# Performance work log

Hardware: AMD Instinct MI355X
Metric: run time of the kernel (lower is better)

Reference implementation:

```python
import jax, jax.numpy as jnp
import numpy as np

D_MODEL = 1024

def setup_inputs() -> dict:
    key = jax.random.key(0)
    k1, k2, kU, kb, kw, kfb = jax.random.split(key, 6)
    B, S, d = 8, 2048, D_MODEL
    x1 = jax.random.normal(k1, (B, S, d), dtype=jnp.float32)
    x2 = jax.random.normal(k2, (B, S, d), dtype=jnp.float32)
    U = jax.random.normal(kU, (d, d), dtype=jnp.float32) * (1.0 / np.sqrt(d))
    bias = jax.random.normal(kb, (d,), dtype=jnp.float32) * 0.02
    fc_w = jax.random.normal(kw, (d // 2, d), dtype=jnp.float32) * (1.0 / np.sqrt(d))
    fc_b = jnp.zeros((d // 2,), dtype=jnp.float32)
    return {"x1": x1, "x2": x2, "U": U, "bias": bias, "fc_w": fc_w, "fc_b": fc_b}

def reference(x1, x2, U, bias, fc_w, fc_b):
    # attn scores: (x2 @ U) @ x1^T  -> [B, S2, S1]
    attn = jnp.einsum("bsd,de,bte->bst", x2, U, x1)
    # additive bias per key position: x1 @ bias -> [B, 1, S1]
    attn = attn + jnp.einsum("btd,d->bt", x1, bias)[:, None, :]
    attn = jax.nn.softmax(attn, axis=-1)
    # dropout is identity in eval mode
    out = jnp.einsum("bst,btd->bsd", attn, x1)
    out = jnp.einsum("bsd,ed->bse", out, fc_w) + fc_b
    return jax.nn.relu(out)
```

## Files before the change

kernel.cpp:

```cpp
#include <hip/hip_runtime.h>
#include <hip/hip_fp16.h>
#include <cstddef>
#include <cstdint>

typedef _Float16 f16;
typedef _Float16 f16x8 __attribute__((ext_vector_type(8)));
typedef _Float16 f16x4 __attribute__((ext_vector_type(4)));
typedef float    f32x4 __attribute__((ext_vector_type(4)));

#define BK 64

__device__ __forceinline__ void gload16(const void* g, void* lds) {
  __builtin_amdgcn_global_load_lds(
      (const __attribute__((address_space(1))) unsigned int*)g,
      (__attribute__((address_space(3))) unsigned int*)lds, 16, 0, 0);
}

template<int R>
__device__ __forceinline__ void stage_f16(f16 (*buf)[BK], const f16* __restrict__ src,
                                          int ld, int w, int lane) {
#pragma unroll
  for (int i = 0; i < R / 32; i++) {
    const int grp  = w * (R / 32) + i;
    const int r    = grp * 8 + (lane >> 3);
    const int slot = (lane & 7) ^ (r & 7);
    gload16(src + (size_t)r * ld + slot * 8, &buf[grp * 8][0]);
  }
}

template<int R>
struct RegStage {
  static constexpr int NV = (R == 128) ? 8 : 4;
  float4 v[NV];
  __device__ __forceinline__ void load(const float* __restrict__ src, int ld, int tid) {
    const int r = (R == 128) ? (tid >> 1) : (tid >> 2);
    const int h = (R == 128) ? (tid & 1) * 32 : (tid & 3) * 16;
    const float* p = src + (size_t)r * ld + h;
#pragma unroll
    for (int j = 0; j < NV; j++) v[j] = ((const float4*)p)[j];
  }
  __device__ __forceinline__ void write(f16 (*buf)[BK], int tid) {
    const int r = (R == 128) ? (tid >> 1) : (tid >> 2);
    const int h = (R == 128) ? (tid & 1) * 32 : (tid & 3) * 16;
#pragma unroll
    for (int g = 0; g < NV / 2; g++) {
      const float4 a = v[g * 2], b = v[g * 2 + 1];
      f16x8 o;
      o[0] = (f16)a.x; o[1] = (f16)a.y; o[2] = (f16)a.z; o[3] = (f16)a.w;
      o[4] = (f16)b.x; o[5] = (f16)b.y; o[6] = (f16)b.z; o[7] = (f16)b.w;
      const int slot = (h / 8 + g) ^ (r & 7);
      *(f16x8*)&buf[r][slot * 8] = o;
    }
  }
};

template<int BMt, int BNt, typename TA, typename TB, bool BIAS, bool RELU, typename TC>
__global__ __launch_bounds__(256, 2)
void gemm_tn(const TA* __restrict__ A, int lda,
             const TB* __restrict__ B, int ldb,
             TC* __restrict__ C, int ldc,
             const float* __restrict__ bias, int K)
{
  constexpr int MF = BMt / 32;
  constexpr int NF = BNt / 32;
  __shared__ f16 As[2][BMt][BK];
  __shared__ f16 Bs[2][BNt][BK];
  const int tid  = threadIdx.x;
  const int lane = tid & 63;
  const int w    = tid >> 6;
  const int wr   = w >> 1, wc = w & 1;

  const int gx = gridDim.x, nxy = gx * gridDim.y;
  int lin = blockIdx.y * gx + blockIdx.x;
  lin = (lin & 7) * (nxy >> 3) + (lin >> 3);
  const int m0 = (lin % gx) * BMt;
  const int n0 = (lin / gx) * BNt;

  f32x4 acc[MF][NF] = {};
  RegStage<BMt> ra;
  RegStage<BNt> rb;

  auto stage_issue = [&](int buf, int k0) {
    if constexpr (sizeof(TA) == 2)
      stage_f16<BMt>(As[buf], (const f16*)A + (size_t)m0 * lda + k0, lda, w, lane);
    else
      ra.load((const float*)A + (size_t)m0 * lda + k0, lda, tid);
    if constexpr (sizeof(TB) == 2)
      stage_f16<BNt>(Bs[buf], (const f16*)B + (size_t)n0 * ldb + k0, ldb, w, lane);
    else
      rb.load((const float*)B + (size_t)n0 * ldb + k0, ldb, tid);
  };
  auto stage_write = [&](int buf) {
    if constexpr (sizeof(TA) == 4) ra.write(As[buf], tid);
    if constexpr (sizeof(TB) == 4) rb.write(Bs[buf], tid);
  };
  auto compute = [&](int buf) {
    const int fr = lane & 15, q = lane >> 4;
#pragma unroll
    for (int kk = 0; kk < 2; kk++) {
      f16x8 af[MF], bf[NF];
#pragma unroll
      for (int i = 0; i < MF; i++) {
        const int r = wr * (BMt / 2) + i * 16 + fr;
        const int slot = (kk * 4 + q) ^ (r & 7);
        af[i] = *(const f16x8*)&As[buf][r][slot * 8];
      }
#pragma unroll
      for (int j = 0; j < NF; j++) {
        const int r = wc * (BNt / 2) + j * 16 + fr;
        const int slot = (kk * 4 + q) ^ (r & 7);
        bf[j] = *(const f16x8*)&Bs[buf][r][slot * 8];
      }
#pragma unroll
      for (int i = 0; i < MF; i++)
#pragma unroll
        for (int j = 0; j < NF; j++)
          acc[i][j] = __builtin_amdgcn_mfma_f32_16x16x32_f16(af[i], bf[j], acc[i][j], 0, 0, 0);
    }
  };

  stage_issue(0, 0);
  stage_write(0);
  __syncthreads();

  const int KT = K / BK;
  for (int kt = 0; kt < KT; kt++) {
    const int cur = kt & 1, nxt = cur ^ 1;
    if (kt + 1 < KT) stage_issue(nxt, (kt + 1) * BK);
    compute(cur);
    if (kt + 1 < KT) stage_write(nxt);
    __syncthreads();
  }

  const int fr = lane & 15;
  const int rg = (lane >> 4) << 2;
#pragma unroll
  for (int i = 0; i < MF; i++) {
#pragma unroll
    for (int j = 0; j < NF; j++) {
      const int col = n0 + wc * (BNt / 2) + j * 16 + fr;
      float bv = 0.f;
      if constexpr (BIAS) bv = bias[col];
#pragma unroll
      for (int r = 0; r < 4; r++) {
        const int row = m0 + wr * (BMt / 2) + i * 16 + rg + r;
        float v = acc[i][j][r] + bv;
        if constexpr (RELU) v = fmaxf(v, 0.f);
        C[(size_t)row * ldc + col] = (TC)v;
      }
    }
  }
}

__global__ __launch_bounds__(256)
void copy_f32_f16(const float* __restrict__ in, f16* __restrict__ o)
{
  const size_t i = ((size_t)blockIdx.x * 256 + threadIdx.x) * 8;
  const float4 a = ((const float4*)(in + i))[0];
  const float4 b = ((const float4*)(in + i))[1];
  f16x8 v;
  v[0] = (f16)a.x; v[1] = (f16)a.y; v[2] = (f16)a.z; v[3] = (f16)a.w;
  v[4] = (f16)b.x; v[5] = (f16)b.y; v[6] = (f16)b.z; v[7] = (f16)b.w;
  *(f16x8*)(o + i) = v;
}

__global__ __launch_bounds__(256)
void copy_uf(const float* __restrict__ U, const float* __restrict__ fcw,
             f16* __restrict__ Uh, f16* __restrict__ Fh)
{
  const bool isU = blockIdx.x < 512;
  const size_t base = (size_t)(isU ? blockIdx.x : blockIdx.x - 512) * 2048;
  const float* in = (isU ? U : fcw) + base;
  f16* o = (isU ? Uh : Fh) + base;
  const size_t i = (size_t)threadIdx.x * 8;
  const float4 a = ((const float4*)(in + i))[0];
  const float4 b = ((const float4*)(in + i))[1];
  f16x8 v;
  v[0] = (f16)a.x; v[1] = (f16)a.y; v[2] = (f16)a.z; v[3] = (f16)a.w;
  v[4] = (f16)b.x; v[5] = (f16)b.y; v[6] = (f16)b.z; v[7] = (f16)b.w;
  *(f16x8*)(o + i) = v;
}

__global__ __launch_bounds__(256)
void bias_dot(const float* __restrict__ x1, const float* __restrict__ bias,
              float* __restrict__ bT)
{
  const int row  = blockIdx.x * 4 + (threadIdx.x >> 6);
  const int lane = threadIdx.x & 63;
  const float4* r = (const float4*)(x1 + (size_t)row * 1024);
  const float4* bb = (const float4*)bias;
  float acc = 0.f;
#pragma unroll
  for (int j = 0; j < 4; j++) {
    const float4 a = r[lane + j * 64];
    const float4 b = bb[lane + j * 64];
    acc += a.x * b.x + a.y * b.y + a.z * b.z + a.w * b.w;
  }
#pragma unroll
  for (int off = 32; off > 0; off >>= 1) acc += __shfl_xor(acc, off);
  if (lane == 0) bT[row] = acc;
}

__global__ __launch_bounds__(256)
void softmax_rows(float* __restrict__ S)
{
  float* row = S + (size_t)blockIdx.x * 2048;
  const int t = threadIdx.x;
  const float4 v0 = ((const float4*)row)[t];
  const float4 v1 = ((const float4*)row)[t + 256];

  float m = fmaxf(fmaxf(fmaxf(v0.x, v0.y), fmaxf(v0.z, v0.w)),
                  fmaxf(fmaxf(v1.x, v1.y), fmaxf(v1.z, v1.w)));
#pragma unroll
  for (int off = 32; off > 0; off >>= 1) m = fmaxf(m, __shfl_xor(m, off));
  __shared__ float red[8];
  if ((t & 63) == 0) red[t >> 6] = m;
  __syncthreads();
  m = fmaxf(fmaxf(red[0], red[1]), fmaxf(red[2], red[3]));

  float e0 = __expf(v0.x - m), e1 = __expf(v0.y - m), e2 = __expf(v0.z - m), e3 = __expf(v0.w - m);
  float e4 = __expf(v1.x - m), e5 = __expf(v1.y - m), e6 = __expf(v1.z - m), e7 = __expf(v1.w - m);
  float s = ((e0 + e1) + (e2 + e3)) + ((e4 + e5) + (e6 + e7));
#pragma unroll
  for (int off = 32; off > 0; off >>= 1) s += __shfl_xor(s, off);
  if ((t & 63) == 0) red[4 + (t >> 6)] = s;
  __syncthreads();
  const float inv = 1.f / (red[4] + red[5] + red[6] + red[7]);

  f16x4 o0, o1;
  o0[0] = (f16)(e0 * inv); o0[1] = (f16)(e1 * inv); o0[2] = (f16)(e2 * inv); o0[3] = (f16)(e3 * inv);
  o1[0] = (f16)(e4 * inv); o1[1] = (f16)(e5 * inv); o1[2] = (f16)(e6 * inv); o1[3] = (f16)(e7 * inv);
  f16x4* orow = (f16x4*)row;
  orow[t]       = o0;
  orow[t + 256] = o1;
}

extern "C" void kernel_launch(void* const* d_in, const int* in_sizes, int n_in,
                              void* d_out, int out_size, void* d_ws, size_t ws_size,
                              hipStream_t stream)
{
  const float* x1   = (const float*)d_in[0];
  const float* x2   = (const float*)d_in[1];
  const float* U    = (const float*)d_in[2];
  const float* bias = (const float*)d_in[3];
  const float* fcw  = (const float*)d_in[4];
  const float* fcb  = (const float*)d_in[5];
  float* out = (float*)d_out;

  const int S = 2048, D = 1024, E = 512, B = 8;
  const size_t MB = 1ull << 20;
  const size_t KB64 = 64 * 1024;

  const bool FULL = ws_size >= (4 * MB + KB64 + 16 * MB);

  char* w = (char*)d_ws;
  f16*   W2   = (f16*)(w);
  f16*   W1Tf = (f16*)(w + 4 * MB);
  float* bT   = FULL ? (float*)(w + 4 * MB) : (float*)(w + 6 * MB);
  float* Sb   = FULL ? (float*)(w + 4 * MB + KB64) : (float*)(w + 6 * MB + KB64);
  f16*   Uh   = FULL ? (f16*)((char*)Sb + 13 * MB) : (f16*)(w + 14 * MB + KB64);
  f16*   Fh   = (f16*)(w + 16 * MB + KB64);
  f16*   W1T  = FULL ? (f16*)Sb + 2048 : W1Tf;
  const int ldw1t = FULL ? 2 * S : S;

  f16* X2h = (f16*)d_out;

  copy_f32_f16<<<dim3(B * S * D / 2048), 256, 0, stream>>>(x2, X2h);
  bias_dot<<<dim3(B * S / 4), 256, 0, stream>>>(x1, bias, bT);
  if (!FULL)
    copy_uf<<<dim3(768), 256, 0, stream>>>(U, fcw, Uh, Fh);

  for (int b = 0; b < B; b++) {
    const float* x1b = x1 + (size_t)b * S * D;
    const f16*   X2b = X2h + (size_t)b * S * D;

    if (FULL) {
      copy_uf<<<dim3(512), 256, 0, stream>>>(U, fcw, Uh, nullptr);

      gemm_tn<64, 128, float, f16, false, false, f16><<<dim3(S / 64, D / 128), 256, 0, stream>>>(
          x1b, D, Uh, D, W2, D, nullptr, D);

      gemm_tn<128, 128, f16, f16, true, false, float><<<dim3(S / 128, S / 128), 256, 0, stream>>>(
          X2b, D, W2, D, Sb, S, bT + (size_t)b * S, D);

      softmax_rows<<<dim3(S), 256, 0, stream>>>(Sb);

      gemm_tn<64, 64, float, float, false, false, f16><<<dim3(E / 64, S / 64), 256, 0, stream>>>(
          fcw, D, x1b, D, W1T, ldw1t, nullptr, D);

      gemm_tn<64, 64, f16, f16, true, true, float><<<dim3(S / 64, E / 64), 256, 0, stream>>>(
          (const f16*)Sb, 2 * S, W1T, ldw1t, out + (size_t)b * S * E, E, fcb, S);
    } else {
      gemm_tn<64, 128, float, f16, false, false, f16><<<dim3(S / 64, D / 128), 256, 0, stream>>>(
          x1b, D, Uh, D, W2, D, nullptr, D);
      gemm_tn<64, 64, f16, float, false, false, f16><<<dim3(E / 64, S / 64), 256, 0, stream>>>(
          Fh, D, x1b, D, W1Tf, S, nullptr, D);
      for (int s0 = 0; s0 < S; s0 += 1024) {
        gemm_tn<64, 128, f16, f16, true, false, float><<<dim3(1024 / 64, S / 128), 256, 0, stream>>>(
            X2b + (size_t)s0 * D, D, W2, D, Sb, S, bT + (size_t)b * S, D);
        softmax_rows<<<dim3(1024), 256, 0, stream>>>(Sb);
        gemm_tn<64, 64, f16, f16, true, true, float><<<dim3(1024 / 64, E / 64), 256, 0, stream>>>(
            (const f16*)Sb, 2 * S, W1Tf, S, out + ((size_t)b * S + s0) * E, E, fcb, S);
      }
    }
  }
}
```

Baseline: 721.5 us.

## Fuse prep kernels, hoist U conversion, use wave-per-row softmax

Merges the x2 fp16 conversion and the bias dot product into one launch. Adds a workspace mode that gives Uh its own slot so the U conversion runs once instead of once per batch. Replaces the block-per-row softmax with a wave-per-row version that reduces only with shuffles and needs no shared memory or barriers. The main savings are fewer launches and no block-level synchronisation in softmax. The cost is higher register pressure in softmax (32 floats per lane) and a more complex workspace layout.

```diff
diff --git a/kernel.cpp b/kernel.cpp
--- a/kernel.cpp
+++ b/kernel.cpp
@@ -153,6 +153,37 @@
 }
 
 __global__ __launch_bounds__(256)
+void prep_head(const float* __restrict__ x2, f16* __restrict__ X2h,
+               const float* __restrict__ x1, const float* __restrict__ bias,
+               float* __restrict__ bT)
+{
+  if (blockIdx.x < 8192) {
+    const size_t i = ((size_t)blockIdx.x * 256 + threadIdx.x) * 8;
+    const float4 a = ((const float4*)(x2 + i))[0];
+    const float4 b = ((const float4*)(x2 + i))[1];
+    f16x8 v;
+    v[0] = (f16)a.x; v[1] = (f16)a.y; v[2] = (f16)a.z; v[3] = (f16)a.w;
+    v[4] = (f16)b.x; v[5] = (f16)b.y; v[6] = (f16)b.z; v[7] = (f16)b.w;
+    *(f16x8*)(X2h + i) = v;
+  } else {
+    const int row  = (blockIdx.x - 8192) * 4 + (threadIdx.x >> 6);
+    const int lane = threadIdx.x & 63;
+    const float4* r = (const float4*)(x1 + (size_t)row * 1024);
+    const float4* bb = (const float4*)bias;
+    float acc = 0.f;
+#pragma unroll
+    for (int j = 0; j < 4; j++) {
+      const float4 a = r[lane + j * 64];
+      const float4 b = bb[lane + j * 64];
+      acc += a.x * b.x + a.y * b.y + a.z * b.z + a.w * b.w;
+    }
+#pragma unroll
+    for (int off = 32; off > 0; off >>= 1) acc += __shfl_xor(acc, off);
+    if (lane == 0) bT[row] = acc;
+  }
+}
+
+__global__ __launch_bounds__(256)
 void copy_f32_f16(const float* __restrict__ in, f16* __restrict__ o)
 {
   const size_t i = ((size_t)blockIdx.x * 256 + threadIdx.x) * 8;
@@ -182,57 +213,39 @@
 }
 
 __global__ __launch_bounds__(256)
-void bias_dot(const float* __restrict__ x1, const float* __restrict__ bias,
-              float* __restrict__ bT)
+void softmax_rows_w(float* __restrict__ S)
 {
   const int row  = blockIdx.x * 4 + (threadIdx.x >> 6);
   const int lane = threadIdx.x & 63;
-  const float4* r = (const float4*)(x1 + (size_t)row * 1024);
-  const float4* bb = (const float4*)bias;
-  float acc = 0.f;
-#pragma unroll
-  for (int j = 0; j < 4; j++) {
-    const float4 a = r[lane + j * 64];
-    const float4 b = bb[lane + j * 64];
-    acc += a.x * b.x + a.y * b.y + a.z * b.z + a.w * b.w;
-  }
-#pragma unroll
-  for (int off = 32; off > 0; off >>= 1) acc += __shfl_xor(acc, off);
-  if (lane == 0) bT[row] = acc;
-}
-
-__global__ __launch_bounds__(256)
-void softmax_rows(float* __restrict__ S)
-{
-  float* row = S + (size_t)blockIdx.x * 2048;
-  const int t = threadIdx.x;
-  const float4 v0 = ((const float4*)row)[t];
-  const float4 v1 = ((const float4*)row)[t + 256];
-
-  float m = fmaxf(fmaxf(fmaxf(v0.x, v0.y), fmaxf(v0.z, v0.w)),
-                  fmaxf(fmaxf(v1.x, v1.y), fmaxf(v1.z, v1.w)));
+  float* rp = S + (size_t)row * 2048;
+  const float4* pr = (const float4*)rp + lane;
+
+  float f[32];
+  float m = -3.4e38f;
+#pragma unroll
+  for (int k = 0; k < 8; k++) {
+    const float4 v = pr[(size_t)k * 64];
+    f[k * 4 + 0] = v.x; f[k * 4 + 1] = v.y; f[k * 4 + 2] = v.z; f[k * 4 + 3] = v.w;
+    m = fmaxf(m, fmaxf(fmaxf(v.x, v.y), fmaxf(v.z, v.w)));
+  }
 #pragma unroll
   for (int off = 32; off > 0; off >>= 1) m = fmaxf(m, __shfl_xor(m, off));
-  __shared__ float red[8];
-  if ((t & 63) == 0) red[t >> 6] = m;
-  __syncthreads();
-  m = fmaxf(fmaxf(red[0], red[1]), fmaxf(red[2], red[3]));
-
-  float e0 = __expf(v0.x - m), e1 = __expf(v0.y - m), e2 = __expf(v0.z - m), e3 = __expf(v0.w - m);
-  float e4 = __expf(v1.x - m), e5 = __expf(v1.y - m), e6 = __expf(v1.z - m), e7 = __expf(v1.w - m);
-  float s = ((e0 + e1) + (e2 + e3)) + ((e4 + e5) + (e6 + e7));
+
+  float s = 0.f;
+#pragma unroll
+  for (int i = 0; i < 32; i++) { f[i] = __expf(f[i] - m); s += f[i]; }
 #pragma unroll
   for (int off = 32; off > 0; off >>= 1) s += __shfl_xor(s, off);
-  if ((t & 63) == 0) red[4 + (t >> 6)] = s;
-  __syncthreads();
-  const float inv = 1.f / (red[4] + red[5] + red[6] + red[7]);
-
-  f16x4 o0, o1;
-  o0[0] = (f16)(e0 * inv); o0[1] = (f16)(e1 * inv); o0[2] = (f16)(e2 * inv); o0[3] = (f16)(e3 * inv);
-  o1[0] = (f16)(e4 * inv); o1[1] = (f16)(e5 * inv); o1[2] = (f16)(e6 * inv); o1[3] = (f16)(e7 * inv);
-  f16x4* orow = (f16x4*)row;
-  orow[t]       = o0;
-  orow[t + 256] = o1;
+  const float inv = 1.f / s;
+
+  f16* hp = (f16*)rp;
+#pragma unroll
+  for (int k = 0; k < 8; k++) {
+    f16x4 o;
+    o[0] = (f16)(f[k * 4 + 0] * inv); o[1] = (f16)(f[k * 4 + 1] * inv);
+    o[2] = (f16)(f[k * 4 + 2] * inv); o[3] = (f16)(f[k * 4 + 3] * inv);
+    *(f16x4*)(hp + 4 * lane + 256 * k) = o;
+  }
 }
 
 extern "C" void kernel_launch(void* const* d_in, const int* in_sizes, int n_in,
@@ -251,31 +264,38 @@
   const size_t MB = 1ull << 20;
   const size_t KB64 = 64 * 1024;
 
-  const bool FULL = ws_size >= (4 * MB + KB64 + 16 * MB);
+  const int MODE = (ws_size >= 4 * MB + KB64 + 2 * MB + 16 * MB) ? 2
+                 : (ws_size >= 4 * MB + KB64 + 16 * MB)          ? 1 : 0;
 
   char* w = (char*)d_ws;
   f16*   W2   = (f16*)(w);
   f16*   W1Tf = (f16*)(w + 4 * MB);
-  float* bT   = FULL ? (float*)(w + 4 * MB) : (float*)(w + 6 * MB);
-  float* Sb   = FULL ? (float*)(w + 4 * MB + KB64) : (float*)(w + 6 * MB + KB64);
-  f16*   Uh   = FULL ? (f16*)((char*)Sb + 13 * MB) : (f16*)(w + 14 * MB + KB64);
+  float* bT   = MODE ? (float*)(w + 4 * MB) : (float*)(w + 6 * MB);
+  float* Sb   = (MODE == 2) ? (float*)(w + 6 * MB + KB64)
+              : MODE        ? (float*)(w + 4 * MB + KB64)
+                            : (float*)(w + 6 * MB + KB64);
+  f16*   Uh   = (MODE == 2) ? (f16*)(w + 4 * MB + KB64)
+              : MODE        ? (f16*)((char*)Sb + 13 * MB)
+                            : (f16*)(w + 14 * MB + KB64);
   f16*   Fh   = (f16*)(w + 16 * MB + KB64);
-  f16*   W1T  = FULL ? (f16*)Sb + 2048 : W1Tf;
-  const int ldw1t = FULL ? 2 * S : S;
+  f16*   W1T  = MODE ? (f16*)Sb + 2048 : W1Tf;
+  const int ldw1t = MODE ? 2 * S : S;
 
   f16* X2h = (f16*)d_out;
 
-  copy_f32_f16<<<dim3(B * S * D / 2048), 256, 0, stream>>>(x2, X2h);
-  bias_dot<<<dim3(B * S / 4), 256, 0, stream>>>(x1, bias, bT);
-  if (!FULL)
+  prep_head<<<dim3(8192 + 4096), 256, 0, stream>>>(x2, X2h, x1, bias, bT);
+  if (MODE == 2)
+    copy_uf<<<dim3(512), 256, 0, stream>>>(U, fcw, Uh, nullptr);
+  else if (MODE == 0)
     copy_uf<<<dim3(768), 256, 0, stream>>>(U, fcw, Uh, Fh);
 
   for (int b = 0; b < B; b++) {
     const float* x1b = x1 + (size_t)b * S * D;
     const f16*   X2b = X2h + (size_t)b * S * D;
 
-    if (FULL) {
-      copy_uf<<<dim3(512), 256, 0, stream>>>(U, fcw, Uh, nullptr);
+    if (MODE) {
+      if (MODE == 1)
+        copy_uf<<<dim3(512), 256, 0, stream>>>(U, fcw, Uh, nullptr);
 
       gemm_tn<64, 128, float, f16, false, false, f16><<<dim3(S / 64, D / 128), 256, 0, stream>>>(
           x1b, D, Uh, D, W2, D, nullptr, D);
@@ -283,7 +303,7 @@
       gemm_tn<128, 128, f16, f16, true, false, float><<<dim3(S / 128, S / 128), 256, 0, stream>>>(
           X2b, D, W2, D, Sb, S, bT + (size_t)b * S, D);
 
-      softmax_rows<<<dim3(S), 256, 0, stream>>>(Sb);
+      softmax_rows_w<<<dim3(S / 4), 256, 0, stream>>>(Sb);
 
       gemm_tn<64, 64, float, float, false, false, f16><<<dim3(E / 64, S / 64), 256, 0, stream>>>(
           fcw, D, x1b, D, W1T, ldw1t, nullptr, D);
@@ -298,7 +318,7 @@
       for (int s0 = 0; s0 < S; s0 += 1024) {
         gemm_tn<64, 128, f16, f16, true, false, float><<<dim3(1024 / 64, S / 128), 256, 0, stream>>>(
             X2b + (size_t)s0 * D, D, W2, D, Sb, S, bT + (size_t)b * S, D);
-        softmax_rows<<<dim3(1024), 256, 0, stream>>>(Sb);
+        softmax_rows_w<<<dim3(1024 / 4), 256, 0, stream>>>(Sb);
         gemm_tn<64, 64, f16, f16, true, true, float><<<dim3(1024 / 64, E / 64), 256, 0, stream>>>(
             (const f16*)Sb, 2 * S, W1Tf, S, out + ((size_t)b * S + s0) * E, E, fcb, S);
       }
```

Result: faster. 700.5 us, median of 2 (-2.9%).
